# Optimization experiments

Measured on AMD Instinct MI355X. Metric: run time of the kernel, lower is better.

## Reference

```python
import jax, jax.numpy as jnp
import numpy as np

KERNEL_SIZE = 5
GROUP_SIZE = 1
SCALE = 2


def setup_inputs() -> dict:
    key = jax.random.key(0)
    k1, k2 = jax.random.split(key)
    N, C, H, W = 2, 256, 100, 100
    features = jax.random.normal(k1, (N, C, H, W), dtype=jnp.float32)
    masks = jax.random.uniform(
        k2, (N, KERNEL_SIZE * KERNEL_SIZE * GROUP_SIZE, H * SCALE, W * SCALE),
        dtype=jnp.float32)
    return {"features": features, "masks": masks}


def _carafe_naive(features, masks, k, g, s):
    N, C, H, W = features.shape
    r = (k - 1) // 2
    # zero-pad spatially, then gather the k*k neighborhood of every low-res pixel
    pad = jnp.pad(features, ((0, 0), (0, 0), (r, r), (r, r)))
    # patches: [N, C, k*k, H, W] -- fixed small loop over k*k shifts
    patches = jnp.stack(
        [pad[:, :, dy:dy + H, dx:dx + W] for dy in range(k) for dx in range(k)],
        axis=2)
    cg = C // g
    # masks: [N, g, k*k, H, s, W, s]  (output pixel (h*s+a, w*s+b))
    m = masks.reshape(N, g, k * k, H, s, W, s)
    # patches per group: [N, g, cg, k*k, H, W]
    p = patches.reshape(N, g, cg, k * k, H, W)
    # weighted sum over the k*k window; result [N, g, cg, H, s, W, s]
    out = jnp.einsum('ngkhawb,ngckhw->ngchawb', m, p)
    return out.reshape(N, C, H * s, W * s)


def reference(features, masks):
    return _carafe_naive(features, masks, KERNEL_SIZE, GROUP_SIZE, SCALE)
```

## Files before the change

### kernel.cpp

```cpp
#include <hip/hip_runtime.h>


typedef float v2f __attribute__((ext_vector_type(2)));
typedef float v4f __attribute__((ext_vector_type(4)));

#define N_ 2
#define C_ 256
#define H_ 100
#define W_ 100
#define HW_ (H_ * W_)
#define OW_ (W_ * 2)
#define OHW_ (HW_ * 4)
#define TS 8
#define HT 12
#define NT 13
#define RSTR 13
#define QOFF (HT * RSTR)
#define WSZ (2 * QOFF)

__global__ __launch_bounds__(256) void carafe_kernel(
    const float* __restrict__ feat,
    const float* __restrict__ mask,
    float* __restrict__ out) {

    __shared__ v4f lds[4 * WSZ];

    const int t    = threadIdx.x;
    const int wv   = t >> 6;
    const int lane = t & 63;
    const int chunk = blockIdx.x * 4 + wv;
    const int ti = blockIdx.y;
    const int n  = blockIdx.z;
    const int tx = ti % NT, ty = ti / NT;
    const int x0 = tx * TS, y0 = ty * TS;

    v4f* wl = lds + wv * WSZ;
    const float* fb = feat + (n * C_ + chunk * 8) * HW_;

#pragma unroll
    for (int r = 0; r < 5; ++r) {
        const int i = r * 64 + lane;
        if (i < 2 * HT * HT) {
            const int q   = i / (HT * HT);
            const int rem = i % (HT * HT);
            const int y   = rem / HT;
            const int col = rem % HT;
            const int yy = y0 - 2 + y;
            const int xx = x0 - 2 + col;
            v4f v = {0.f, 0.f, 0.f, 0.f};
            if (((unsigned)yy < (unsigned)H_) & ((unsigned)xx < (unsigned)W_)) {
                const int o = (q * 4) * HW_ + yy * W_ + xx;
                v.x = fb[o];
                v.y = fb[o + HW_];
                v.z = fb[o + 2 * HW_];
                v.w = fb[o + 3 * HW_];
            }
            wl[q * QOFF + y * RSTR + col] = v;
        }
    }
    asm volatile("s_waitcnt lgkmcnt(0)" ::: "memory");

    const int py = lane >> 3, px = lane & 7;
    const int h  = y0 + py, wpix = x0 + px;
    const bool alive = (h < H_) & (wpix < W_);
    const int hc = min(h, H_ - 1), wc = min(wpix, W_ - 1);
    const int oh0 = 2 * hc, ow0 = 2 * wc;
    const float* mbase = mask + n * (25 * OHW_) + oh0 * OW_ + ow0;

    v2f a0[8], a1[8];
#pragma unroll
    for (int c = 0; c < 8; ++c) { a0[c] = (v2f){0.f, 0.f}; a1[c] = (v2f){0.f, 0.f}; }

#pragma unroll 2
    for (int dy = 0; dy < 5; ++dy) {
        const float* mrow = mbase + (dy * 5) * OHW_;
        const int rb = (py + dy) * RSTR + px;
#pragma unroll
        for (int dx = 0; dx < 5; ++dx) {
            const v2f m0 = *reinterpret_cast<const v2f*>(mrow + dx * OHW_);
            const v2f m1 = *reinterpret_cast<const v2f*>(mrow + dx * OHW_ + OW_);
            const v4f lo = wl[rb + dx];
            const v4f hi = wl[QOFF + rb + dx];
            const float f[8] = {lo.x, lo.y, lo.z, lo.w, hi.x, hi.y, hi.z, hi.w};
#pragma unroll
            for (int c = 0; c < 8; ++c) {
                const v2f fv = {f[c], f[c]};
                a0[c] = __builtin_elementwise_fma(fv, m0, a0[c]);
                a1[c] = __builtin_elementwise_fma(fv, m1, a1[c]);
            }
        }
    }

    if (alive) {
        float* ob = out + (n * C_ + chunk * 8) * OHW_ + oh0 * OW_ + ow0;
#pragma unroll
        for (int c = 0; c < 8; ++c) {
            *reinterpret_cast<v2f*>(ob + c * OHW_)       = a0[c];
            *reinterpret_cast<v2f*>(ob + c * OHW_ + OW_) = a1[c];
        }
    }
}

extern "C" void kernel_launch(void* const* d_in, const int* in_sizes, int n_in,
                              void* d_out, int out_size, void* d_ws, size_t ws_size,
                              hipStream_t stream) {
    const float* feat = (const float*)d_in[0];
    const float* mask = (const float*)d_in[1];
    float* out = (float*)d_out;

    dim3 grid(8, NT * NT, N_);
    carafe_kernel<<<grid, 256, 0, stream>>>(feat, mask, out);
}
```

Baseline: 42.12 us.

## Stage mask tile in shared LDS across all block waves

Each block now loads its 25-tap mask tile once into shared LDS and uses __syncthreads, instead of every wave reading the mask from global memory on its own. Feature staging becomes block-wide, with 32 channels in LDS that the four waves share. The inner loop does v4f FMAs against a 2x2 mask quad. The aim is to cut redundant global mask traffic by four times, at the cost of more LDS use (about 40KB), a block barrier, and possible loss of occupancy.

New measurement: 53.07 us. +26.0%, slower.

```diff
diff --git a/kernel.cpp b/kernel.cpp
--- a/kernel.cpp
+++ b/kernel.cpp
@@ -10,93 +10,111 @@
 #define W_ 100
 #define HW_ (H_ * W_)
 #define OW_ (W_ * 2)
+#define OH_ (H_ * 2)
 #define OHW_ (HW_ * 4)
 #define TS 8
 #define HT 12
 #define NT 13
-#define RSTR 13
-#define QOFF (HT * RSTR)
-#define WSZ (2 * QOFF)
+#define FSTR 13
+#define FQ (HT * FSTR)
+#define NCG 8
 
 __global__ __launch_bounds__(256) void carafe_kernel(
     const float* __restrict__ feat,
     const float* __restrict__ mask,
     float* __restrict__ out) {
 
-    __shared__ v4f lds[4 * WSZ];
+    __shared__ v4f lmq[25 * 64];
+    __shared__ v4f lf4[8 * FQ];
 
-    const int t    = threadIdx.x;
-    const int wv   = t >> 6;
-    const int lane = t & 63;
-    const int chunk = blockIdx.x * 4 + wv;
-    const int ti = blockIdx.y;
-    const int n  = blockIdx.z;
+    const int cg   = blockIdx.x;
+    const int ti   = blockIdx.y;
+    const int n    = blockIdx.z;
     const int tx = ti % NT, ty = ti / NT;
     const int x0 = tx * TS, y0 = ty * TS;
+    const int t = threadIdx.x;
 
-    v4f* wl = lds + wv * WSZ;
-    const float* fb = feat + (n * C_ + chunk * 8) * HW_;
+    {
+        const float* mb = mask + n * (25 * OHW_);
+#pragma unroll
+        for (int r = 0; r < 7; ++r) {
+            const int i = r * 256 + t;
+            if (i < 25 * 64) {
+                const int tap = i >> 6;
+                const int pl  = i & 63;
+                const int py = pl >> 3, px = pl & 7;
+                const int oh = 2 * (y0 + py);
+                const int ow = 2 * (x0 + px);
+                v4f v = {0.f, 0.f, 0.f, 0.f};
+                if ((oh < OH_) & (ow < OW_)) {
+                    const float* p = mb + tap * OHW_ + oh * OW_ + ow;
+                    const v2f r0 = *reinterpret_cast<const v2f*>(p);
+                    const v2f r1 = *reinterpret_cast<const v2f*>(p + OW_);
+                    v = (v4f){r0.x, r0.y, r1.x, r1.y};
+                }
+                lmq[i] = v;
+            }
+        }
+    }
+    {
+        const float* fb = feat + (n * C_ + cg * 32) * HW_;
+#pragma unroll
+        for (int r = 0; r < 5; ++r) {
+            const int j = r * 256 + t;
+            if (j < 8 * HT * HT) {
+                const int q   = j / (HT * HT);
+                const int rem = j % (HT * HT);
+                const int y = rem / HT, x = rem % HT;
+                const int yy = y0 - 2 + y;
+                const int xx = x0 - 2 + x;
+                v4f v = {0.f, 0.f, 0.f, 0.f};
+                if (((unsigned)yy < (unsigned)H_) & ((unsigned)xx < (unsigned)W_)) {
+                    const int o = (q * 4) * HW_ + yy * W_ + xx;
+                    v.x = fb[o];
+                    v.y = fb[o + HW_];
+                    v.z = fb[o + 2 * HW_];
+                    v.w = fb[o + 3 * HW_];
+                }
+                lf4[q * FSTR * HT + y * FSTR + x] = v;
+            }
+        }
+    }
+    __syncthreads();
+
+    const int wv = t >> 6;
+    const int lane = t & 63;
+    const int py = lane >> 3, px = lane & 7;
+    const int q0 = 2 * wv, q1 = 2 * wv + 1;
+
+    v4f acc[8];
+#pragma unroll
+    for (int c = 0; c < 8; ++c) acc[c] = (v4f){0.f, 0.f, 0.f, 0.f};
 
 #pragma unroll
-    for (int r = 0; r < 5; ++r) {
-        const int i = r * 64 + lane;
-        if (i < 2 * HT * HT) {
-            const int q   = i / (HT * HT);
-            const int rem = i % (HT * HT);
-            const int y   = rem / HT;
-            const int col = rem % HT;
-            const int yy = y0 - 2 + y;
-            const int xx = x0 - 2 + col;
-            v4f v = {0.f, 0.f, 0.f, 0.f};
-            if (((unsigned)yy < (unsigned)H_) & ((unsigned)xx < (unsigned)W_)) {
-                const int o = (q * 4) * HW_ + yy * W_ + xx;
-                v.x = fb[o];
-                v.y = fb[o + HW_];
-                v.z = fb[o + 2 * HW_];
-                v.w = fb[o + 3 * HW_];
-            }
-            wl[q * QOFF + y * RSTR + col] = v;
-        }
-    }
-    asm volatile("s_waitcnt lgkmcnt(0)" ::: "memory");
-
-    const int py = lane >> 3, px = lane & 7;
-    const int h  = y0 + py, wpix = x0 + px;
-    const bool alive = (h < H_) & (wpix < W_);
-    const int hc = min(h, H_ - 1), wc = min(wpix, W_ - 1);
-    const int oh0 = 2 * hc, ow0 = 2 * wc;
-    const float* mbase = mask + n * (25 * OHW_) + oh0 * OW_ + ow0;
-
-    v2f a0[8], a1[8];
-#pragma unroll
-    for (int c = 0; c < 8; ++c) { a0[c] = (v2f){0.f, 0.f}; a1[c] = (v2f){0.f, 0.f}; }
-
-#pragma unroll 2
     for (int dy = 0; dy < 5; ++dy) {
-        const float* mrow = mbase + (dy * 5) * OHW_;
-        const int rb = (py + dy) * RSTR + px;
 #pragma unroll
         for (int dx = 0; dx < 5; ++dx) {
-            const v2f m0 = *reinterpret_cast<const v2f*>(mrow + dx * OHW_);
-            const v2f m1 = *reinterpret_cast<const v2f*>(mrow + dx * OHW_ + OW_);
-            const v4f lo = wl[rb + dx];
-            const v4f hi = wl[QOFF + rb + dx];
-            const float f[8] = {lo.x, lo.y, lo.z, lo.w, hi.x, hi.y, hi.z, hi.w};
+            const int tap = dy * 5 + dx;
+            const v4f mq = lmq[tap * 64 + lane];
+            const v4f f0 = lf4[q0 * FQ + (py + dy) * FSTR + (px + dx)];
+            const v4f f1 = lf4[q1 * FQ + (py + dy) * FSTR + (px + dx)];
 #pragma unroll
-            for (int c = 0; c < 8; ++c) {
-                const v2f fv = {f[c], f[c]};
-                a0[c] = __builtin_elementwise_fma(fv, m0, a0[c]);
-                a1[c] = __builtin_elementwise_fma(fv, m1, a1[c]);
+            for (int k = 0; k < 4; ++k) {
+                const v4f s0 = {f0[k], f0[k], f0[k], f0[k]};
+                const v4f s1 = {f1[k], f1[k], f1[k], f1[k]};
+                acc[k]     = __builtin_elementwise_fma(s0, mq, acc[k]);
+                acc[4 + k] = __builtin_elementwise_fma(s1, mq, acc[4 + k]);
             }
         }
     }
 
-    if (alive) {
-        float* ob = out + (n * C_ + chunk * 8) * OHW_ + oh0 * OW_ + ow0;
+    const int h = y0 + py, w = x0 + px;
+    if ((h < H_) & (w < W_)) {
+        float* ob = out + ((n * C_ + cg * 32 + wv * 8) * OHW_) + (2 * h) * OW_ + 2 * w;
 #pragma unroll
         for (int c = 0; c < 8; ++c) {
-            *reinterpret_cast<v2f*>(ob + c * OHW_)       = a0[c];
-            *reinterpret_cast<v2f*>(ob + c * OHW_ + OW_) = a1[c];
+            *reinterpret_cast<v2f*>(ob + c * OHW_)       = (v2f){acc[c].x, acc[c].y};
+            *reinterpret_cast<v2f*>(ob + c * OHW_ + OW_) = (v2f){acc[c].z, acc[c].w};
         }
     }
 }
@@ -108,6 +126,6 @@
     const float* mask = (const float*)d_in[1];
     float* out = (float*)d_out;
 
-    dim3 grid(8, NT * NT, N_);
+    dim3 grid(NCG, NT * NT, N_);
     carafe_kernel<<<grid, 256, 0, stream>>>(feat, mask, out);
 }
```
